# Kernel optimization log

Measured on AMD Instinct MI355X. Metric: run time of the kernel, lower is better.

## Reference

```python
import jax, jax.numpy as jnp
import numpy as np
import math

E = 1024
H = 16
D = E // H  # head_dim = 64
B, T = 2, 2048


def setup_inputs() -> dict:
    key = jax.random.key(0)
    ks = jax.random.split(key, 10)
    s_in = 1.0 / math.sqrt(E)
    s_hd = 1.0 / math.sqrt(D)
    return {
        "hidden_states": jax.random.normal(ks[0], (B, T, E), dtype=jnp.float32),
        # stacked per-head Linear weights (torch Linear: y = x @ W.T + b)
        "Wq": jax.random.uniform(ks[1], (H, E, D), jnp.float32, -s_in, s_in),
        "bq": jax.random.uniform(ks[2], (H, D), jnp.float32, -s_in, s_in),
        "Wk": jax.random.uniform(ks[3], (H, E, D), jnp.float32, -s_in, s_in),
        "bk": jax.random.uniform(ks[4], (H, D), jnp.float32, -s_in, s_in),
        "Wv": jax.random.uniform(ks[5], (H, E, D), jnp.float32, -s_in, s_in),
        "bv": jax.random.uniform(ks[6], (H, D), jnp.float32, -s_in, s_in),
        "Wo": jax.random.uniform(ks[7], (H, D, E), jnp.float32, -s_hd, s_hd),
        "bo": jax.random.uniform(ks[8], (H, E), jnp.float32, -s_hd, s_hd),
        "gate": jnp.ones((H,), dtype=jnp.float32),
    }


def reference(hidden_states, Wq, bq, Wk, bk, Wv, bv, Wo, bo, gate):
    # Batched per-head projections: [B,T,E] x [H,E,D] -> [B,H,T,D]
    Q = jnp.einsum("bte,hed->bhtd", hidden_states, Wq) + bq[None, :, None, :]
    K = jnp.einsum("bte,hed->bhtd", hidden_states, Wk) + bk[None, :, None, :]
    V = jnp.einsum("bte,hed->bhtd", hidden_states, Wv) + bv[None, :, None, :]
    scale = 1.0 / math.sqrt(D)
    scores = jnp.einsum("bhtd,bhsd->bhts", Q, K) * scale  # [B,H,T,T]
    weights = jax.nn.softmax(scores, axis=-1)
    attn = jnp.einsum("bhts,bhsd->bhtd", weights, V)  # [B,H,T,D]
    # Per-head output proj (bias included before gating), gated, summed over heads
    proj = jnp.einsum("bhtd,hde->bhte", attn, Wo) + bo[None, :, None, :]
    out = jnp.sum(proj * gate[None, :, None, None], axis=1)  # [B,T,E]
    return out
```

## Files before the change

### kernel.cpp

```cpp
#include <hip/hip_runtime.h>
#include <math.h>

#define E_DIM 1024
#define H_DIM 16
#define D_DIM 64
#define B_DIM 2
#define T_DIM 2048
#define M_TOT (B_DIM * T_DIM)

typedef __bf16 bf16_t;
typedef bf16_t bf16x2 __attribute__((ext_vector_type(2)));
typedef bf16_t bf16x4 __attribute__((ext_vector_type(4)));
typedef bf16_t bf16x8 __attribute__((ext_vector_type(8)));
typedef float f32x4 __attribute__((ext_vector_type(4)));
typedef float f32x16 __attribute__((ext_vector_type(16)));
typedef unsigned int uint4v __attribute__((ext_vector_type(4)));

#define LOG2E_DIV8 0.18033688011112042f

__device__ __forceinline__ float fast_exp2(float x) {
#if __has_builtin(__builtin_amdgcn_exp2f)
    return __builtin_amdgcn_exp2f(x);
#else
    return __expf(x * 0.6931471805599453f);
#endif
}

__device__ __forceinline__ unsigned pack_bf16x2(float a, float b) {
    bf16x2 t = {(bf16_t)a, (bf16_t)b};
    return __builtin_bit_cast(unsigned, t);
}

__device__ __forceinline__ void swap32(unsigned& a, unsigned& b, int hi) {
    unsigned as = (unsigned)__shfl_xor((int)a, 32);
    unsigned bs = (unsigned)__shfl_xor((int)b, 32);
    unsigned na = hi ? bs : a;
    unsigned nb = hi ? b : as;
    a = na; b = nb;
}

__device__ __forceinline__ void load_lds16(const void* g, void* l) {
    __builtin_amdgcn_global_load_lds(
        (const __attribute__((address_space(1))) unsigned int*)g,
        (__attribute__((address_space(3))) unsigned int*)l, 16, 0, 0);
}

__global__ __launch_bounds__(256) void prep_kernel(
    const float* __restrict__ x,
    const float* __restrict__ Wq, const float* __restrict__ Wk,
    const float* __restrict__ Wv, const float* __restrict__ Wo,
    const float* __restrict__ bo, const float* __restrict__ gate,
    bf16_t* __restrict__ Xb, bf16_t* __restrict__ Wcat,
    bf16_t* __restrict__ Wgt, float* __restrict__ bsum) {
    __shared__ float Tt[64][65];
    const int b = blockIdx.x;
    const int tid = threadIdx.x;

    if (b < 2048) {
        size_t i = ((size_t)b * 256 + tid) * 8;
        float4 a0 = *reinterpret_cast<const float4*>(x + i);
        float4 a1 = *reinterpret_cast<const float4*>(x + i + 4);
        bf16x8 o;
        o[0] = (bf16_t)a0.x; o[1] = (bf16_t)a0.y; o[2] = (bf16_t)a0.z; o[3] = (bf16_t)a0.w;
        o[4] = (bf16_t)a1.x; o[5] = (bf16_t)a1.y; o[6] = (bf16_t)a1.z; o[7] = (bf16_t)a1.w;
        *reinterpret_cast<bf16x8*>(Xb + i) = o;
    } else if (b < 2816) {
        const int idx = b - 2048;
        const int z = idx >> 8;
        const int rem = idx & 255;
        const int h = rem >> 4, et = rem & 15;
        const float* W = z == 0 ? Wq : (z == 1 ? Wk : Wv);
        const int r = tid >> 2, c4 = (tid & 3) * 16;
        const float* src = W + (size_t)h * 65536 + (size_t)(et * 64 + r) * 64 + c4;
        #pragma unroll
        for (int k = 0; k < 16; k += 4) {
            float4 v = *reinterpret_cast<const float4*>(src + k);
            Tt[r][c4 + k + 0] = v.x; Tt[r][c4 + k + 1] = v.y;
            Tt[r][c4 + k + 2] = v.z; Tt[r][c4 + k + 3] = v.w;
        }
        __syncthreads();
        bf16x8 o0, o1;
        #pragma unroll
        for (int k = 0; k < 8; ++k) o0[k] = (bf16_t)Tt[c4 + k][r];
        #pragma unroll
        for (int k = 0; k < 8; ++k) o1[k] = (bf16_t)Tt[c4 + 8 + k][r];
        bf16_t* dst = Wcat + ((size_t)(z * 16 + h) * 64 + r) * 1024 + et * 64 + c4;
        *reinterpret_cast<bf16x8*>(dst) = o0;
        *reinterpret_cast<bf16x8*>(dst + 8) = o1;
    } else if (b < 3072) {
        const int idx = b - 2816;
        const int h = idx >> 4, et = idx & 15;
        const float g = gate[h];
        const int r = tid >> 2, c4 = (tid & 3) * 16;
        const float* src = Wo + (size_t)h * 65536 + (size_t)r * 1024 + et * 64 + c4;
        #pragma unroll
        for (int k = 0; k < 16; k += 4) {
            float4 v = *reinterpret_cast<const float4*>(src + k);
            Tt[r][c4 + k + 0] = v.x * g; Tt[r][c4 + k + 1] = v.y * g;
            Tt[r][c4 + k + 2] = v.z * g; Tt[r][c4 + k + 3] = v.w * g;
        }
        __syncthreads();
        bf16x8 o0, o1;
        #pragma unroll
        for (int k = 0; k < 8; ++k) o0[k] = (bf16_t)Tt[c4 + k][r];
        #pragma unroll
        for (int k = 0; k < 8; ++k) o1[k] = (bf16_t)Tt[c4 + 8 + k][r];
        bf16_t* dst = Wgt + (size_t)(et * 64 + r) * 1024 + h * 64 + c4;
        *reinterpret_cast<bf16x8*>(dst) = o0;
        *reinterpret_cast<bf16x8*>(dst + 8) = o1;
    } else {
        const int e = (b - 3072) * 256 + tid;
        float s = 0.f;
        #pragma unroll
        for (int h = 0; h < H_DIM; ++h) s += gate[h] * bo[h * E_DIM + e];
        bsum[e] = s;
    }
}

__global__ __launch_bounds__(256) void qkv_gemm_kernel(
    const bf16_t* __restrict__ Xb, const bf16_t* __restrict__ Wcat,
    const float* __restrict__ bqp, const float* __restrict__ bkp,
    const float* __restrict__ bvp,
    bf16_t* __restrict__ Qw, bf16_t* __restrict__ Kw, bf16_t* __restrict__ Vtw) {
    const int p = blockIdx.x;
    const int l = (p & 7) * 96 + (p >> 3);
    const int mx = l & 31, ny = l >> 5;
    const int m0 = mx * 128, n0 = ny * 128;
    const int z = n0 >> 10;

    __shared__ bf16_t As[128][32];
    __shared__ bf16_t Bs[128][32];

    const int tid = threadIdx.x;
    const int lane = tid & 63, wid = tid >> 6;
    const int wr = wid >> 1, wc = wid & 1;
    const int lr = lane & 15, lg = lane >> 4;
    const int srow = lane >> 2, scol = (lane & 3) * 8;

    const int b_idx = m0 >> 11;
    const int t00 = m0 & (T_DIM - 1);

    #define QKV_STAGE(k0)                                                          \
        _Pragma("unroll")                                                          \
        for (int j = 0; j < 2; ++j) {                                              \
            load_lds16(Xb + (size_t)(m0 + wid * 32 + j * 16 + srow) * E_DIM + (k0) + scol, \
                       (char*)&As[0][0] + wid * 2048 + j * 1024);                  \
            load_lds16(Wcat + (size_t)(n0 + wid * 32 + j * 16 + srow) * E_DIM + (k0) + scol, \
                       (char*)&Bs[0][0] + wid * 2048 + j * 1024);                  \
        }
    #define QKV_FRAGS                                                              \
        bf16x8 a[4], bb[4];                                                        \
        _Pragma("unroll")                                                          \
        for (int i = 0; i < 4; ++i)                                                \
            a[i] = *reinterpret_cast<const bf16x8*>(&As[wr * 64 + i * 16 + lr][lg * 8]); \
        _Pragma("unroll")                                                          \
        for (int j = 0; j < 4; ++j)                                                \
            bb[j] = *reinterpret_cast<const bf16x8*>(&Bs[wc * 64 + j * 16 + lr][lg * 8]);

    if (z < 2) {
        f32x4 acc[4][4] = {};
        for (int k0 = 0; k0 < E_DIM; k0 += 32) {
            QKV_STAGE(k0);
            __syncthreads();
            QKV_FRAGS;
            __builtin_amdgcn_s_setprio(1);
            #pragma unroll
            for (int j = 0; j < 4; ++j)
                #pragma unroll
                for (int i = 0; i < 4; ++i)
                    acc[j][i] = __builtin_amdgcn_mfma_f32_16x16x32_bf16(bb[j], a[i], acc[j][i], 0, 0, 0);
            __builtin_amdgcn_s_setprio(0);
            __syncthreads();
        }
        const float scale = (z == 0) ? LOG2E_DIV8 : 1.0f;
        const float* bias = (z == 0) ? bqp : bkp;
        bf16_t* Obase = (z == 0) ? Qw : Kw;
        #pragma unroll
        for (int j = 0; j < 4; ++j) {
            const int n = n0 + wc * 64 + j * 16 + lg * 4;
            const int h = (n >> 6) & 15;
            const int dbase = n & 63;
            const float4 bv4 = *reinterpret_cast<const float4*>(&bias[n & 1023]);
            bf16_t* O = Obase + (size_t)(b_idx * H_DIM + h) * T_DIM * 64;
            #pragma unroll
            for (int i = 0; i < 4; ++i) {
                const int t = t00 + wr * 64 + i * 16 + lr;
                bf16x4 t4;
                #pragma unroll
                for (int r = 0; r < 4; ++r)
                    t4[r] = (bf16_t)((acc[j][i][r] + (&bv4.x)[r]) * scale);
                *reinterpret_cast<bf16x4*>(&O[(size_t)t * 64 + dbase]) = t4;
            }
        }
    } else {
        f32x4 acc[4][4] = {};
        for (int k0 = 0; k0 < E_DIM; k0 += 32) {
            QKV_STAGE(k0);
            __syncthreads();
            QKV_FRAGS;
            __builtin_amdgcn_s_setprio(1);
            #pragma unroll
            for (int i = 0; i < 4; ++i)
                #pragma unroll
                for (int j = 0; j < 4; ++j)
                    acc[i][j] = __builtin_amdgcn_mfma_f32_16x16x32_bf16(a[i], bb[j], acc[i][j], 0, 0, 0);
            __builtin_amdgcn_s_setprio(0);
            __syncthreads();
        }
        #pragma unroll
        for (int j = 0; j < 4; ++j) {
            const int n = n0 + wc * 64 + j * 16 + lr;
            const int h = (n >> 6) & 15;
            const int d = n & 63;
            const float bval = bvp[n & 1023];
            bf16_t* O = Vtw + (size_t)(b_idx * H_DIM + h) * 64 * T_DIM + (size_t)d * T_DIM;
            #pragma unroll
            for (int i = 0; i < 4; ++i) {
                const int t = t00 + wr * 64 + i * 16 + lg * 4;
                bf16x4 t4;
                #pragma unroll
                for (int r = 0; r < 4; ++r) t4[r] = (bf16_t)(acc[i][j][r] + bval);
                *reinterpret_cast<bf16x4*>(&O[t]) = t4;
            }
        }
    }
    #undef QKV_STAGE
    #undef QKV_FRAGS
}

__global__ __launch_bounds__(256, 3) void attn_mfma_kernel(
    const bf16_t* __restrict__ Q, const bf16_t* __restrict__ K,
    const bf16_t* __restrict__ Vt, bf16_t* __restrict__ Aw) {
    const int p = blockIdx.x;
    const int l = (p & 7) * 64 + (p >> 3);
    const int qx = l & 15, bh = l >> 4;
    const int b_idx = bh >> 4, h = bh & 15;
    const int q0 = qx * 128;
    const size_t base = (size_t)bh * T_DIM * 64;

    __shared__ bf16_t Ks[64][72];
    __shared__ bf16_t Vs[64][72];

    const int tid = threadIdx.x;
    const int lane = tid & 63;
    const int w = tid >> 6;
    const int lq = lane & 31;
    const int hi = lane >> 5;

    const int qrow = q0 + w * 32 + lq;
    bf16x8 qb[4];
    #pragma unroll
    for (int kc = 0; kc < 4; ++kc)
        qb[kc] = *reinterpret_cast<const bf16x8*>(
            Q + base + (size_t)qrow * 64 + kc * 16 + hi * 8);

    const int sr = tid >> 2, sc = (tid & 3) * 16;

    float mreg = -INFINITY, lrow = 0.f;
    f32x16 o[2] = {};

    for (int s0 = 0; s0 < T_DIM; s0 += 64) {
        {
            const bf16_t* ksrc = K + base + (size_t)(s0 + sr) * 64 + sc;
            bf16x8 k0 = *reinterpret_cast<const bf16x8*>(ksrc);
            bf16x8 k1 = *reinterpret_cast<const bf16x8*>(ksrc + 8);
            const bf16_t* vsrc = Vt + base + (size_t)sr * T_DIM + s0 + sc;
            bf16x8 v0 = *reinterpret_cast<const bf16x8*>(vsrc);
            bf16x8 v1 = *reinterpret_cast<const bf16x8*>(vsrc + 8);
            *reinterpret_cast<bf16x8*>(&Ks[sr][sc])     = k0;
            *reinterpret_cast<bf16x8*>(&Ks[sr][sc + 8]) = k1;
            *reinterpret_cast<bf16x8*>(&Vs[sr][sc])     = v0;
            *reinterpret_cast<bf16x8*>(&Vs[sr][sc + 8]) = v1;
        }
        __syncthreads();

        f32x16 s32[2] = {};
        __builtin_amdgcn_s_setprio(1);
        #pragma unroll
        for (int sb = 0; sb < 2; ++sb)
            #pragma unroll
            for (int kc = 0; kc < 4; ++kc) {
                bf16x8 ka = *reinterpret_cast<const bf16x8*>(
                    &Ks[sb * 32 + lq][kc * 16 + hi * 8]);
                s32[sb] = __builtin_amdgcn_mfma_f32_32x32x16_bf16(ka, qb[kc], s32[sb], 0, 0, 0);
            }
        __builtin_amdgcn_s_setprio(0);

        float pmax = -INFINITY;
        #pragma unroll
        for (int sb = 0; sb < 2; ++sb)
            #pragma unroll
            for (int r = 0; r < 16; r += 4)
                pmax = fmaxf(pmax, fmaxf(fmaxf(s32[sb][r], s32[sb][r + 1]),
                                         fmaxf(s32[sb][r + 2], s32[sb][r + 3])));
        pmax = fmaxf(pmax, __shfl_xor(pmax, 32));

        if (__any(pmax > mreg + 11.5f)) {
            float newm = fmaxf(mreg, pmax);
            float alpha = fast_exp2(mreg - newm);
            mreg = newm;
            lrow *= alpha;
            o[0] *= alpha;
            o[1] *= alpha;
        }

        float rs = 0.f;
        unsigned W[2][4][2];
        #pragma unroll
        for (int sb = 0; sb < 2; ++sb)
            #pragma unroll
            for (int grp = 0; grp < 4; ++grp) {
                float p0 = fast_exp2(s32[sb][grp * 4 + 0] - mreg);
                float p1 = fast_exp2(s32[sb][grp * 4 + 1] - mreg);
                float p2 = fast_exp2(s32[sb][grp * 4 + 2] - mreg);
                float p3 = fast_exp2(s32[sb][grp * 4 + 3] - mreg);
                rs += (p0 + p1) + (p2 + p3);
                W[sb][grp][0] = pack_bf16x2(p0, p1);
                W[sb][grp][1] = pack_bf16x2(p2, p3);
            }
        rs += __shfl_xor(rs, 32);
        lrow += rs;

        bf16x8 pa[4];
        #pragma unroll
        for (int sb = 0; sb < 2; ++sb)
            #pragma unroll
            for (int kl = 0; kl < 2; ++kl) {
                unsigned a0 = W[sb][2 * kl][0], b0 = W[sb][2 * kl + 1][0];
                unsigned a1 = W[sb][2 * kl][1], b1 = W[sb][2 * kl + 1][1];
                swap32(a0, b0, hi);
                swap32(a1, b1, hi);
                uint4v tv = {a0, a1, b0, b1};
                pa[sb * 2 + kl] = __builtin_bit_cast(bf16x8, tv);
            }

        __builtin_amdgcn_s_setprio(1);
        #pragma unroll
        for (int ks = 0; ks < 4; ++ks)
            #pragma unroll
            for (int db = 0; db < 2; ++db) {
                bf16x8 va = *reinterpret_cast<const bf16x8*>(
                    &Vs[db * 32 + lq][ks * 16 + hi * 8]);
                o[db] = __builtin_amdgcn_mfma_f32_32x32x16_bf16(va, pa[ks], o[db], 0, 0, 0);
            }
        __builtin_amdgcn_s_setprio(0);
        __syncthreads();
    }

    const float linv = 1.f / lrow;
    const size_t rowbase = ((size_t)b_idx * T_DIM + qrow) * E_DIM + h * 64;
    #pragma unroll
    for (int db = 0; db < 2; ++db)
        #pragma unroll
        for (int grp = 0; grp < 4; ++grp) {
            bf16x4 t4;
            #pragma unroll
            for (int i = 0; i < 4; ++i)
                t4[i] = (bf16_t)(o[db][grp * 4 + i] * linv);
            *reinterpret_cast<bf16x4*>(
                &Aw[rowbase + db * 32 + grp * 8 + hi * 4]) = t4;
        }
}

__global__ __launch_bounds__(256) void out_gemm_kernel(
    const bf16_t* __restrict__ Aw, const bf16_t* __restrict__ Wgt,
    const float* __restrict__ bsum, float* __restrict__ out) {
    const int p = blockIdx.x;
    const int l = (p & 7) * 64 + (p >> 3);
    const int mx = l & 31, ny = l >> 5;
    const int m0 = mx * 128, n0 = ny * 64;

    __shared__ bf16_t As[128][32];
    __shared__ bf16_t Bs[64][32];

    const int tid = threadIdx.x;
    const int lane = tid & 63, wid = tid >> 6;
    const int wr = wid >> 1, wc = wid & 1;
    const int lr = lane & 15, lg = lane >> 4;
    const int srow = lane >> 2, scol = (lane & 3) * 8;

    f32x4 acc[2][4] = {};

    for (int k0 = 0; k0 < E_DIM; k0 += 32) {
        #pragma unroll
        for (int j = 0; j < 2; ++j)
            load_lds16(Aw + (size_t)(m0 + wid * 32 + j * 16 + srow) * E_DIM + k0 + scol,
                       (char*)&As[0][0] + wid * 2048 + j * 1024);
        load_lds16(Wgt + (size_t)(n0 + wid * 16 + srow) * E_DIM + k0 + scol,
                   (char*)&Bs[0][0] + wid * 1024);
        __syncthreads();
        bf16x8 a[4], bb[2];
        #pragma unroll
        for (int i = 0; i < 4; ++i)
            a[i] = *reinterpret_cast<const bf16x8*>(&As[wr * 64 + i * 16 + lr][lg * 8]);
        #pragma unroll
        for (int j = 0; j < 2; ++j)
            bb[j] = *reinterpret_cast<const bf16x8*>(&Bs[wc * 32 + j * 16 + lr][lg * 8]);
        __builtin_amdgcn_s_setprio(1);
        #pragma unroll
        for (int j = 0; j < 2; ++j)
            #pragma unroll
            for (int i = 0; i < 4; ++i)
                acc[j][i] = __builtin_amdgcn_mfma_f32_16x16x32_bf16(bb[j], a[i], acc[j][i], 0, 0, 0);
        __builtin_amdgcn_s_setprio(0);
        __syncthreads();
    }

    #pragma unroll
    for (int j = 0; j < 2; ++j) {
        const int e = n0 + wc * 32 + j * 16 + lg * 4;
        const float4 bs4 = *reinterpret_cast<const float4*>(&bsum[e]);
        #pragma unroll
        for (int i = 0; i < 4; ++i) {
            const int m = m0 + wr * 64 + i * 16 + lr;
            float4 o4;
            o4.x = acc[j][i][0] + bs4.x;
            o4.y = acc[j][i][1] + bs4.y;
            o4.z = acc[j][i][2] + bs4.z;
            o4.w = acc[j][i][3] + bs4.w;
            *reinterpret_cast<float4*>(&out[(size_t)m * E_DIM + e]) = o4;
        }
    }
}

extern "C" void kernel_launch(void* const* d_in, const int* in_sizes, int n_in,
                              void* d_out, int out_size, void* d_ws, size_t ws_size,
                              hipStream_t stream) {
    const float* hs   = (const float*)d_in[0];
    const float* Wq   = (const float*)d_in[1];
    const float* bq   = (const float*)d_in[2];
    const float* Wk   = (const float*)d_in[3];
    const float* bk   = (const float*)d_in[4];
    const float* Wv   = (const float*)d_in[5];
    const float* bv   = (const float*)d_in[6];
    const float* Wo   = (const float*)d_in[7];
    const float* bo   = (const float*)d_in[8];
    const float* gate = (const float*)d_in[9];
    float* out = (float*)d_out;

    const size_t NX = (size_t)M_TOT * E_DIM;
    const size_t NW = (size_t)H_DIM * D_DIM * E_DIM;
    bf16_t* p = (bf16_t*)d_ws;
    bf16_t* Xb   = p; p += NX;
    bf16_t* Wcat = p; p += 3 * NW;
    bf16_t* Wgt  = p; p += NW;
    bf16_t* Qw   = p; p += NX;
    bf16_t* Kw   = p; p += NX;
    bf16_t* Vtw  = p; p += NX;
    bf16_t* Aw   = p; p += NX;
    float*  bsum = (float*)p;

    prep_kernel<<<dim3(3076), 256, 0, stream>>>(hs, Wq, Wk, Wv, Wo, bo, gate,
                                                Xb, Wcat, Wgt, bsum);

    qkv_gemm_kernel<<<dim3(768), 256, 0, stream>>>(Xb, Wcat, bq, bk, bv, Qw, Kw, Vtw);

    attn_mfma_kernel<<<dim3(512), 256, 0, stream>>>(Qw, Kw, Vtw, Aw);

    out_gemm_kernel<<<dim3(512), 256, 0, stream>>>(Aw, Wgt, bsum, out);
}
```

Measured before the change: 203.8 us.

## Double-buffer K/V tiles in LDS and widen attention key tile to 128

The attention kernel now prefetches the next K/V tile into registers while computing on the current one, and writes it into a second LDS buffer after the PV MFMAs. This needs only one barrier per iteration and hides global load latency. The key tile grows from 64 to 128 rows, which halves the number of loop iterations and barriers. In exchange, LDS use and register pressure rise (more score accumulators and prefetch registers), and launch bounds drop from 3 to 2 blocks per SM, reducing occupancy.

Result: faster. 198.1 us (-2.8%).

```diff
diff --git a/kernel.cpp b/kernel.cpp
--- a/kernel.cpp
+++ b/kernel.cpp
@@ -228,7 +228,7 @@
     #undef QKV_FRAGS
 }
 
-__global__ __launch_bounds__(256, 3) void attn_mfma_kernel(
+__global__ __launch_bounds__(256, 2) void attn_mfma_kernel(
     const bf16_t* __restrict__ Q, const bf16_t* __restrict__ K,
     const bf16_t* __restrict__ Vt, bf16_t* __restrict__ Aw) {
     const int p = blockIdx.x;
@@ -238,8 +238,8 @@
     const int q0 = qx * 128;
     const size_t base = (size_t)bh * T_DIM * 64;
 
-    __shared__ bf16_t Ks[64][72];
-    __shared__ bf16_t Vs[64][72];
+    __shared__ bf16_t Ks[2][128][72];
+    __shared__ bf16_t Vs[2][64][136];
 
     const int tid = threadIdx.x;
     const int lane = tid & 63;
@@ -254,41 +254,51 @@
         qb[kc] = *reinterpret_cast<const bf16x8*>(
             Q + base + (size_t)qrow * 64 + kc * 16 + hi * 8);
 
-    const int sr = tid >> 2, sc = (tid & 3) * 16;
+    const int kr = tid >> 1, kc0 = (tid & 1) * 32;
+    const int vr = tid >> 2, vc0 = (tid & 3) * 32;
+
+    bf16x8 kreg[4], vreg[4];
+    #define ATT_LOAD(s0)                                                           \
+        {   const bf16_t* ksrc = K + base + (size_t)((s0) + kr) * 64 + kc0;        \
+            const bf16_t* vsrc = Vt + base + (size_t)vr * T_DIM + (s0) + vc0;      \
+            _Pragma("unroll")                                                      \
+            for (int j = 0; j < 4; ++j) {                                          \
+                kreg[j] = *reinterpret_cast<const bf16x8*>(ksrc + j * 8);          \
+                vreg[j] = *reinterpret_cast<const bf16x8*>(vsrc + j * 8);          \
+            } }
+    #define ATT_WRITE(buf)                                                         \
+        {   _Pragma("unroll")                                                      \
+            for (int j = 0; j < 4; ++j) {                                          \
+                *reinterpret_cast<bf16x8*>(&Ks[buf][kr][kc0 + j * 8]) = kreg[j];   \
+                *reinterpret_cast<bf16x8*>(&Vs[buf][vr][vc0 + j * 8]) = vreg[j];   \
+            } }
+
+    ATT_LOAD(0);
+    ATT_WRITE(0);
+    __syncthreads();
 
     float mreg = -INFINITY, lrow = 0.f;
     f32x16 o[2] = {};
-
-    for (int s0 = 0; s0 < T_DIM; s0 += 64) {
-        {
-            const bf16_t* ksrc = K + base + (size_t)(s0 + sr) * 64 + sc;
-            bf16x8 k0 = *reinterpret_cast<const bf16x8*>(ksrc);
-            bf16x8 k1 = *reinterpret_cast<const bf16x8*>(ksrc + 8);
-            const bf16_t* vsrc = Vt + base + (size_t)sr * T_DIM + s0 + sc;
-            bf16x8 v0 = *reinterpret_cast<const bf16x8*>(vsrc);
-            bf16x8 v1 = *reinterpret_cast<const bf16x8*>(vsrc + 8);
-            *reinterpret_cast<bf16x8*>(&Ks[sr][sc])     = k0;
-            *reinterpret_cast<bf16x8*>(&Ks[sr][sc + 8]) = k1;
-            *reinterpret_cast<bf16x8*>(&Vs[sr][sc])     = v0;
-            *reinterpret_cast<bf16x8*>(&Vs[sr][sc + 8]) = v1;
-        }
-        __syncthreads();
-
-        f32x16 s32[2] = {};
+    int cur = 0;
+
+    for (int it = 0; it < 16; ++it) {
+        if (it < 15) ATT_LOAD((it + 1) * 128);
+
+        f32x16 s32[4] = {};
         __builtin_amdgcn_s_setprio(1);
         #pragma unroll
-        for (int sb = 0; sb < 2; ++sb)
+        for (int sb = 0; sb < 4; ++sb)
             #pragma unroll
             for (int kc = 0; kc < 4; ++kc) {
                 bf16x8 ka = *reinterpret_cast<const bf16x8*>(
-                    &Ks[sb * 32 + lq][kc * 16 + hi * 8]);
+                    &Ks[cur][sb * 32 + lq][kc * 16 + hi * 8]);
                 s32[sb] = __builtin_amdgcn_mfma_f32_32x32x16_bf16(ka, qb[kc], s32[sb], 0, 0, 0);
             }
         __builtin_amdgcn_s_setprio(0);
 
         float pmax = -INFINITY;
         #pragma unroll
-        for (int sb = 0; sb < 2; ++sb)
+        for (int sb = 0; sb < 4; ++sb)
             #pragma unroll
             for (int r = 0; r < 16; r += 4)
                 pmax = fmaxf(pmax, fmaxf(fmaxf(s32[sb][r], s32[sb][r + 1]),
@@ -305,9 +315,10 @@
         }
 
         float rs = 0.f;
-        unsigned W[2][4][2];
-        #pragma unroll
-        for (int sb = 0; sb < 2; ++sb)
+        bf16x8 pa[8];
+        #pragma unroll
+        for (int sb = 0; sb < 4; ++sb) {
+            unsigned Wl[4][2];
             #pragma unroll
             for (int grp = 0; grp < 4; ++grp) {
                 float p0 = fast_exp2(s32[sb][grp * 4 + 0] - mreg);
@@ -315,37 +326,39 @@
                 float p2 = fast_exp2(s32[sb][grp * 4 + 2] - mreg);
                 float p3 = fast_exp2(s32[sb][grp * 4 + 3] - mreg);
                 rs += (p0 + p1) + (p2 + p3);
-                W[sb][grp][0] = pack_bf16x2(p0, p1);
-                W[sb][grp][1] = pack_bf16x2(p2, p3);
-            }
-        rs += __shfl_xor(rs, 32);
-        lrow += rs;
-
-        bf16x8 pa[4];
-        #pragma unroll
-        for (int sb = 0; sb < 2; ++sb)
+                Wl[grp][0] = pack_bf16x2(p0, p1);
+                Wl[grp][1] = pack_bf16x2(p2, p3);
+            }
             #pragma unroll
             for (int kl = 0; kl < 2; ++kl) {
-                unsigned a0 = W[sb][2 * kl][0], b0 = W[sb][2 * kl + 1][0];
-                unsigned a1 = W[sb][2 * kl][1], b1 = W[sb][2 * kl + 1][1];
+                unsigned a0 = Wl[2 * kl][0], b0 = Wl[2 * kl + 1][0];
+                unsigned a1 = Wl[2 * kl][1], b1 = Wl[2 * kl + 1][1];
                 swap32(a0, b0, hi);
                 swap32(a1, b1, hi);
                 uint4v tv = {a0, a1, b0, b1};
                 pa[sb * 2 + kl] = __builtin_bit_cast(bf16x8, tv);
             }
+        }
+        rs += __shfl_xor(rs, 32);
+        lrow += rs;
 
         __builtin_amdgcn_s_setprio(1);
         #pragma unroll
-        for (int ks = 0; ks < 4; ++ks)
+        for (int ks = 0; ks < 8; ++ks)
             #pragma unroll
             for (int db = 0; db < 2; ++db) {
                 bf16x8 va = *reinterpret_cast<const bf16x8*>(
-                    &Vs[db * 32 + lq][ks * 16 + hi * 8]);
+                    &Vs[cur][db * 32 + lq][ks * 16 + hi * 8]);
                 o[db] = __builtin_amdgcn_mfma_f32_32x32x16_bf16(va, pa[ks], o[db], 0, 0, 0);
             }
         __builtin_amdgcn_s_setprio(0);
+
+        if (it < 15) ATT_WRITE(cur ^ 1);
         __syncthreads();
+        cur ^= 1;
     }
+    #undef ATT_LOAD
+    #undef ATT_WRITE
 
     const float linv = 1.f / lrow;
     const size_t rowbase = ((size_t)b_idx * T_DIM + qrow) * E_DIM + h * 64;
```
